# Kernel optimization log

Measured on AMD Instinct MI355X. Metric: run time of the kernel, lower is better.

Reference implementation:

```python
import jax, jax.numpy as jnp
import numpy as np

N_ETYPES = 4


def setup_inputs() -> dict:
    key = jax.random.key(0)
    ks = jax.random.split(key, 6)
    N, E, F = 50000, 800000, 128
    x = jax.random.normal(ks[0], (N, F), dtype=jnp.float32)
    edge_index = jax.random.randint(ks[1], (2, E), 0, N, dtype=jnp.int64)
    edge_type = jax.random.randint(ks[2], (E,), 0, N_ETYPES, dtype=jnp.int64)
    scale = 1.0 / np.sqrt(F)
    W_self = jax.random.normal(ks[3], (N_ETYPES, F, F), dtype=jnp.float32) * scale
    W_neigh = jax.random.normal(ks[4], (N_ETYPES, F, F), dtype=jnp.float32) * scale
    b = jnp.zeros((N_ETYPES, F), dtype=jnp.float32)
    return {"x": x, "edge_index": edge_index, "edge_type": edge_type,
            "W_self": W_self, "W_neigh": W_neigh, "b": b}


def reference(x, edge_index, edge_type, W_self, W_neigh, b):
    # HeteroConv: per-edge-type SageConv (mean aggregation), then mean over types.
    N = x.shape[0]
    src, dst = edge_index[0], edge_index[1]
    msg = x[src]                                   # [E, F] gathered source features
    outs = []
    for t in range(N_ETYPES):                      # small fixed loop over edge types
        w = (edge_type == t).astype(x.dtype)[:, None]          # [E, 1] type mask
        agg = jax.ops.segment_sum(msg * w, dst, num_segments=N)  # [N, F]
        cnt = jax.ops.segment_sum(w, dst, num_segments=N)        # [N, 1]
        mean_agg = agg / jnp.maximum(cnt, 1.0)
        outs.append(x @ W_self[t] + mean_agg @ W_neigh[t] + b[t])
    out = jnp.stack(outs, axis=0)                  # [n_etypes, N, F]
    return out.mean(axis=0)                        # reduction='mean' over edge types
```

## Files before the change

### kernel.cpp

```cpp
#include <hip/hip_runtime.h>

#define FDIM 128
#define NT 4
#define KDIM (FDIM * (NT + 1))
#define GBM 32

#define RSH 5
#define RNODES 32
#define RCAP 768
#define NBKT 128
#define CHUNK 4096

typedef __attribute__((ext_vector_type(8))) _Float16 h8v;
typedef __attribute__((ext_vector_type(4))) float f4v;

__device__ __forceinline__ unsigned short f2h(float f) {
    _Float16 h = (_Float16)f;
    return __builtin_bit_cast(unsigned short, h);
}
__device__ __forceinline__ void gload_lds16(const void* g, void* l) {
    __builtin_amdgcn_global_load_lds(
        (const __attribute__((address_space(1))) unsigned int*)g,
        (__attribute__((address_space(3))) unsigned int*)l, 16, 0, 0);
}

__global__ __launch_bounds__(256) void x2h(const float* __restrict__ x,
                                           unsigned short* __restrict__ xh, int n4) {
    int i = blockIdx.x * blockDim.x + threadIdx.x;
    if (i < n4) {
        float4 v = reinterpret_cast<const float4*>(x)[i];
        ushort4 o;
        o.x = f2h(v.x);
        o.y = f2h(v.y);
        o.z = f2h(v.z);
        o.w = f2h(v.w);
        reinterpret_cast<ushort4*>(xh)[i] = o;
    }
}

__global__ void mix_weights(const float* __restrict__ Wself,
                            const float* __restrict__ Wneigh,
                            const float* __restrict__ b,
                            unsigned short* __restrict__ WmixT,
                            float* __restrict__ bmean) {
    int i = blockIdx.x * blockDim.x + threadIdx.x;
    if (i >= KDIM * FDIM) return;
    int k = i / FDIM, j = i % FDIM;
    float v;
    if (k < FDIM) {
        v = 0.25f * (Wself[(size_t)(0 * FDIM + k) * FDIM + j] +
                     Wself[(size_t)(1 * FDIM + k) * FDIM + j] +
                     Wself[(size_t)(2 * FDIM + k) * FDIM + j] +
                     Wself[(size_t)(3 * FDIM + k) * FDIM + j]);
    } else {
        int t = (k - FDIM) >> 7;
        int kk = (k - FDIM) & (FDIM - 1);
        v = 0.25f * Wneigh[((size_t)t * FDIM + kk) * FDIM + j];
    }
    WmixT[(size_t)j * KDIM + k] = f2h(v);
    if (i < FDIM) {
        bmean[i] = 0.25f * (b[i] + b[FDIM + i] + b[2 * FDIM + i] + b[3 * FDIM + i]);
    }
}

__global__ __launch_bounds__(256) void k_bin(
    const int* __restrict__ ei, const int* __restrict__ et,
    int* __restrict__ cur, unsigned int* __restrict__ bin,
    int N, int E, int NR) {
    __shared__ int lcnt[2048];
    __shared__ int lpos[2048];
    const int tid = threadIdx.x;
    const int e0 = blockIdx.x * CHUNK;

    for (int b = tid; b < NR; b += 256) lcnt[b] = 0;
    __syncthreads();

    int rs[16];
    unsigned int recs[16];
#pragma unroll
    for (int i = 0; i < 16; ++i) {
        int e = e0 + i * 256 + tid;
        if (e < E) {
            int src = ei[e];
            int dst = ei[E + e];
            int t = et[e];
            rs[i] = dst >> RSH;
            recs[i] = (unsigned int)src |
                      ((unsigned int)(dst & (RNODES - 1)) << 16) |
                      ((unsigned int)t << 21);
            atomicAdd(&lcnt[rs[i]], 1);
        } else {
            rs[i] = -1;
            recs[i] = 0;
        }
    }
    __syncthreads();

    for (int b = tid; b < NR; b += 256) {
        int c = lcnt[b];
        lpos[b] = (c > 0) ? atomicAdd(&cur[b * 16], c) : 0;
    }
    __syncthreads();

#pragma unroll
    for (int i = 0; i < 16; ++i) {
        if (rs[i] >= 0) {
            int p = atomicAdd(&lpos[rs[i]], 1);
            if (p < RCAP) bin[(size_t)rs[i] * RCAP + p] = recs[i];
        }
    }
}

__global__ __launch_bounds__(256) void k_fused(
    const unsigned short* __restrict__ xh, const int* __restrict__ cur,
    const unsigned int* __restrict__ bin, const unsigned short* __restrict__ WmixT,
    const float* __restrict__ bmean, float* __restrict__ out, int N) {
    __shared__ __align__(16) char smem[18944];
    unsigned int* recs   = (unsigned int*)smem;
    int* scanb           = (int*)(smem + 3072);
    int* cur2            = (int*)(smem + 3584);
    unsigned short* As   = (unsigned short*)smem;
    unsigned short* magg = (unsigned short*)smem;
    unsigned short* srcs = (unsigned short*)(smem + 8192);
    int* cnts            = (int*)(smem + 9728);
    int* boff            = (int*)(smem + 10240);
    unsigned short* Bs   = (unsigned short*)(smem + 10752);

    const int r = blockIdx.x;
    const int tid = threadIdx.x;

    int K = cur[r * 16];
    if (K > RCAP) K = RCAP;
    for (int i = tid; i < K; i += 256) recs[i] = bin[(size_t)r * RCAP + i];
    if (tid < NBKT) cnts[tid] = 0;
    __syncthreads();
    for (int i = tid; i < K; i += 256) {
        unsigned int rec = recs[i];
        int b = ((rec >> 21) << 5) | ((rec >> 16) & 31);
        atomicAdd(&cnts[b], 1);
    }
    __syncthreads();
    int v = (tid < NBKT) ? cnts[tid] : 0;
    if (tid < NBKT) scanb[tid] = v;
    __syncthreads();
    for (int off = 1; off < NBKT; off <<= 1) {
        int tv = (tid >= off && tid < NBKT) ? scanb[tid - off] : 0;
        __syncthreads();
        if (tid < NBKT) scanb[tid] += tv;
        __syncthreads();
    }
    if (tid < NBKT) { boff[tid] = scanb[tid] - v; cur2[tid] = scanb[tid] - v; }
    __syncthreads();
    for (int i = tid; i < K; i += 256) {
        unsigned int rec = recs[i];
        int b = ((rec >> 21) << 5) | ((rec >> 16) & 31);
        int p = atomicAdd(&cur2[b], 1);
        srcs[p] = (unsigned short)(rec & 0xffffu);
    }

    const int wid = tid >> 6, lane = tid & 63;
    const int wr = wid >> 1, wc = wid & 1;
    const int n0 = r * GBM;
    const int r16 = lane & 15, kg = lane >> 4;
    const int g = tid >> 4, ln = tid & 15;

    f4v acc[4];
#pragma unroll
    for (int n = 0; n < 4; ++n) acc[n] = (f4v){0.f, 0.f, 0.f, 0.f};
    __syncthreads();

#pragma unroll 1
    for (int ks = 0; ks < 4; ++ks) {
        int k0 = ks * 32;
        if (wid < 2) {
            int row = tid >> 2, c = tid & 3;
            int cs = c ^ ((row >> 1) & 3);
            int rg = n0 + row; if (rg >= N) rg = N - 1;
            gload_lds16(xh + (size_t)rg * FDIM + k0 + cs * 8, &As[wid * 512]);
        }
#pragma unroll
        for (int p = 0; p < 2; ++p) {
            int ck = p * 256 + tid;
            int col = ck >> 2, c = ck & 3;
            int cs = c ^ ((col >> 1) & 3);
            gload_lds16(WmixT + (size_t)col * KDIM + k0 + cs * 8,
                        &Bs[(p * 4 + wid) * 512]);
        }
        __syncthreads();
        h8v af, bfr[4];
        {
            int row = wr * 16 + r16;
            af = *reinterpret_cast<const h8v*>(
                &As[row * 32 + ((kg ^ ((row >> 1) & 3)) << 3)]);
        }
#pragma unroll
        for (int n = 0; n < 4; ++n) {
            int col = wc * 64 + n * 16 + r16;
            bfr[n] = *reinterpret_cast<const h8v*>(
                &Bs[col * 32 + ((kg ^ ((col >> 1) & 3)) << 3)]);
        }
#pragma unroll
        for (int n = 0; n < 4; ++n)
            acc[n] = __builtin_amdgcn_mfma_f32_16x16x32_f16(af, bfr[n], acc[n], 0, 0, 0);
        __syncthreads();
    }

#pragma unroll 1
    for (int t = 0; t < 4; ++t) {
#pragma unroll 1
        for (int it = 0; it < 2; ++it) {
            int dl = it * 16 + g;
            int b = (t << 5) | dl;
            int dst = n0 + dl;
            if (dst < N) {
                int beg = boff[b], m = cnts[b];
                h8v a0 = (h8v)(_Float16)0.f, a1 = (h8v)(_Float16)0.f;
                h8v a2 = (h8v)(_Float16)0.f, a3 = (h8v)(_Float16)0.f;
                int i = 0;
                for (; i + 4 <= m; i += 4) {
                    int s0 = srcs[beg + i], s1 = srcs[beg + i + 1];
                    int s2 = srcs[beg + i + 2], s3 = srcs[beg + i + 3];
                    a0 += *reinterpret_cast<const h8v*>(xh + (size_t)s0 * FDIM + ln * 8);
                    a1 += *reinterpret_cast<const h8v*>(xh + (size_t)s1 * FDIM + ln * 8);
                    a2 += *reinterpret_cast<const h8v*>(xh + (size_t)s2 * FDIM + ln * 8);
                    a3 += *reinterpret_cast<const h8v*>(xh + (size_t)s3 * FDIM + ln * 8);
                }
                if (i + 2 <= m) {
                    int s0 = srcs[beg + i], s1 = srcs[beg + i + 1];
                    a0 += *reinterpret_cast<const h8v*>(xh + (size_t)s0 * FDIM + ln * 8);
                    a1 += *reinterpret_cast<const h8v*>(xh + (size_t)s1 * FDIM + ln * 8);
                    i += 2;
                }
                if (i < m) {
                    int s0 = srcs[beg + i];
                    a0 += *reinterpret_cast<const h8v*>(xh + (size_t)s0 * FDIM + ln * 8);
                }
                float rc = (m > 0) ? 1.0f / (float)m : 0.0f;
                h8v o = ((a0 + a1) + (a2 + a3)) * (_Float16)rc;
                *reinterpret_cast<h8v*>(&magg[dl * FDIM + ((ln ^ (dl & 15)) << 3)]) = o;
            }
        }
        __syncthreads();

#pragma unroll 1
        for (int ks = 0; ks < 4; ++ks) {
            int k0 = FDIM + t * FDIM + ks * 32;
#pragma unroll
            for (int p = 0; p < 2; ++p) {
                int ck = p * 256 + tid;
                int col = ck >> 2, c = ck & 3;
                int cs = c ^ ((col >> 1) & 3);
                gload_lds16(WmixT + (size_t)col * KDIM + k0 + cs * 8,
                            &Bs[(p * 4 + wid) * 512]);
            }
            __syncthreads();
            h8v af, bfr[4];
            {
                int row = wr * 16 + r16;
                af = *reinterpret_cast<const h8v*>(
                    &magg[row * FDIM + (((ks * 4 + kg) ^ (row & 15)) << 3)]);
            }
#pragma unroll
            for (int n = 0; n < 4; ++n) {
                int col = wc * 64 + n * 16 + r16;
                bfr[n] = *reinterpret_cast<const h8v*>(
                    &Bs[col * 32 + ((kg ^ ((col >> 1) & 3)) << 3)]);
            }
#pragma unroll
            for (int n = 0; n < 4; ++n)
                acc[n] = __builtin_amdgcn_mfma_f32_16x16x32_f16(af, bfr[n], acc[n], 0, 0, 0);
            __syncthreads();
        }
    }

    float bm[4];
#pragma unroll
    for (int n = 0; n < 4; ++n) bm[n] = bmean[wc * 64 + n * 16 + r16];
#pragma unroll
    for (int j = 0; j < 4; ++j) {
        int row = n0 + wr * 16 + kg * 4 + j;
        if (row < N) {
            float* o = out + (size_t)row * FDIM;
#pragma unroll
            for (int n = 0; n < 4; ++n)
                o[wc * 64 + n * 16 + r16] = acc[n][j] + bm[n];
        }
    }
}

extern "C" void kernel_launch(void* const* d_in, const int* in_sizes, int n_in,
                              void* d_out, int out_size, void* d_ws, size_t ws_size,
                              hipStream_t stream) {
    const float* x      = (const float*)d_in[0];
    const int*   ei     = (const int*)d_in[1];
    const int*   et     = (const int*)d_in[2];
    const float* Wself  = (const float*)d_in[3];
    const float* Wneigh = (const float*)d_in[4];
    const float* b      = (const float*)d_in[5];
    float* out = (float*)d_out;

    const int N = in_sizes[0] / FDIM;
    const int E = in_sizes[2];
    const int NR = (N + RNODES - 1) >> RSH;

    char* ws = (char*)d_ws;
    unsigned short* xh    = (unsigned short*)ws;
    unsigned short* WmixT = xh + (size_t)N * FDIM;
    float* bmean = (float*)(WmixT + (size_t)FDIM * KDIM);
    int* cur     = (int*)(bmean + FDIM);
    unsigned int* bin = (unsigned int*)(cur + (size_t)NR * 16);

    hipMemsetAsync(cur, 0, (size_t)NR * 16 * sizeof(int), stream);

    x2h<<<(N * FDIM / 4 + 255) / 256, 256, 0, stream>>>(x, xh, N * FDIM / 4);

    mix_weights<<<(KDIM * FDIM + 255) / 256, 256, 0, stream>>>(Wself, Wneigh, b, WmixT, bmean);

    k_bin<<<(E + CHUNK - 1) / CHUNK, 256, 0, stream>>>(ei, et, cur, bin, N, E, NR);

    k_fused<<<NR, 256, 0, stream>>>(xh, cur, bin, WmixT, bmean, out, N);
}
```

Measured before the change: 96.25 us.

## Merge prep kernels into one launch and use wave-shuffle bucket scan

The x-to-half conversion, weight mixing and edge binning kernels are merged into one launch that dispatches on block index, removing two kernel launches and letting the three independent prep jobs overlap on the GPU. The x conversion now handles eight elements per thread. In the fused kernel, the 128-bucket prefix scan is replaced by a single-wave shuffle scan with two buckets per lane, which drops several block-wide barriers. The merged kernel reserves the binning kernel's shared-memory footprint for every block, which may reduce occupancy for the conversion blocks.

```diff
diff --git a/kernel.cpp b/kernel.cpp
--- a/kernel.cpp
+++ b/kernel.cpp
@@ -24,89 +24,82 @@
         (__attribute__((address_space(3))) unsigned int*)l, 16, 0, 0);
 }
 
-__global__ __launch_bounds__(256) void x2h(const float* __restrict__ x,
-                                           unsigned short* __restrict__ xh, int n4) {
-    int i = blockIdx.x * blockDim.x + threadIdx.x;
-    if (i < n4) {
-        float4 v = reinterpret_cast<const float4*>(x)[i];
-        ushort4 o;
-        o.x = f2h(v.x);
-        o.y = f2h(v.y);
-        o.z = f2h(v.z);
-        o.w = f2h(v.w);
-        reinterpret_cast<ushort4*>(xh)[i] = o;
-    }
-}
-
-__global__ void mix_weights(const float* __restrict__ Wself,
-                            const float* __restrict__ Wneigh,
-                            const float* __restrict__ b,
-                            unsigned short* __restrict__ WmixT,
-                            float* __restrict__ bmean) {
-    int i = blockIdx.x * blockDim.x + threadIdx.x;
-    if (i >= KDIM * FDIM) return;
-    int k = i / FDIM, j = i % FDIM;
-    float v;
-    if (k < FDIM) {
-        v = 0.25f * (Wself[(size_t)(0 * FDIM + k) * FDIM + j] +
-                     Wself[(size_t)(1 * FDIM + k) * FDIM + j] +
-                     Wself[(size_t)(2 * FDIM + k) * FDIM + j] +
-                     Wself[(size_t)(3 * FDIM + k) * FDIM + j]);
-    } else {
-        int t = (k - FDIM) >> 7;
-        int kk = (k - FDIM) & (FDIM - 1);
-        v = 0.25f * Wneigh[((size_t)t * FDIM + kk) * FDIM + j];
-    }
-    WmixT[(size_t)j * KDIM + k] = f2h(v);
-    if (i < FDIM) {
-        bmean[i] = 0.25f * (b[i] + b[FDIM + i] + b[2 * FDIM + i] + b[3 * FDIM + i]);
-    }
-}
-
-__global__ __launch_bounds__(256) void k_bin(
-    const int* __restrict__ ei, const int* __restrict__ et,
-    int* __restrict__ cur, unsigned int* __restrict__ bin,
-    int N, int E, int NR) {
+__global__ __launch_bounds__(256) void k_prep(
+    const float* __restrict__ x, const int* __restrict__ ei,
+    const int* __restrict__ et, const float* __restrict__ Wself,
+    const float* __restrict__ Wneigh, const float* __restrict__ bvec,
+    unsigned short* __restrict__ xh, unsigned short* __restrict__ WmixT,
+    float* __restrict__ bmean, int* __restrict__ cur,
+    unsigned int* __restrict__ bin, int N, int E, int NR, int nbBin, int nbX) {
     __shared__ int lcnt[2048];
     __shared__ int lpos[2048];
+    const int bid = blockIdx.x;
     const int tid = threadIdx.x;
-    const int e0 = blockIdx.x * CHUNK;
-
-    for (int b = tid; b < NR; b += 256) lcnt[b] = 0;
-    __syncthreads();
-
-    int rs[16];
-    unsigned int recs[16];
-#pragma unroll
-    for (int i = 0; i < 16; ++i) {
-        int e = e0 + i * 256 + tid;
-        if (e < E) {
-            int src = ei[e];
-            int dst = ei[E + e];
-            int t = et[e];
-            rs[i] = dst >> RSH;
-            recs[i] = (unsigned int)src |
-                      ((unsigned int)(dst & (RNODES - 1)) << 16) |
-                      ((unsigned int)t << 21);
-            atomicAdd(&lcnt[rs[i]], 1);
-        } else {
-            rs[i] = -1;
-            recs[i] = 0;
-        }
-    }
-    __syncthreads();
-
-    for (int b = tid; b < NR; b += 256) {
-        int c = lcnt[b];
-        lpos[b] = (c > 0) ? atomicAdd(&cur[b * 16], c) : 0;
-    }
-    __syncthreads();
-
-#pragma unroll
-    for (int i = 0; i < 16; ++i) {
-        if (rs[i] >= 0) {
-            int p = atomicAdd(&lpos[rs[i]], 1);
-            if (p < RCAP) bin[(size_t)rs[i] * RCAP + p] = recs[i];
+
+    if (bid < nbBin) {
+        const int e0 = bid * CHUNK;
+        for (int b = tid; b < NR; b += 256) lcnt[b] = 0;
+        __syncthreads();
+        int rs[16];
+        unsigned int recs[16];
+#pragma unroll
+        for (int i = 0; i < 16; ++i) {
+            int e = e0 + i * 256 + tid;
+            if (e < E) {
+                int src = ei[e];
+                int dst = ei[E + e];
+                int t = et[e];
+                rs[i] = dst >> RSH;
+                recs[i] = (unsigned int)src |
+                          ((unsigned int)(dst & (RNODES - 1)) << 16) |
+                          ((unsigned int)t << 21);
+                atomicAdd(&lcnt[rs[i]], 1);
+            } else { rs[i] = -1; recs[i] = 0; }
+        }
+        __syncthreads();
+        for (int b = tid; b < NR; b += 256) {
+            int c = lcnt[b];
+            lpos[b] = (c > 0) ? atomicAdd(&cur[b * 16], c) : 0;
+        }
+        __syncthreads();
+#pragma unroll
+        for (int i = 0; i < 16; ++i) {
+            if (rs[i] >= 0) {
+                int p = atomicAdd(&lpos[rs[i]], 1);
+                if (p < RCAP) bin[(size_t)rs[i] * RCAP + p] = recs[i];
+            }
+        }
+    } else if (bid < nbBin + nbX) {
+        int i = (bid - nbBin) * 256 + tid;
+        int n8 = N * FDIM / 8;
+        if (i < n8) {
+            float4 v0 = reinterpret_cast<const float4*>(x)[i * 2];
+            float4 v1 = reinterpret_cast<const float4*>(x)[i * 2 + 1];
+            ushort4 o0, o1;
+            o0.x = f2h(v0.x); o0.y = f2h(v0.y); o0.z = f2h(v0.z); o0.w = f2h(v0.w);
+            o1.x = f2h(v1.x); o1.y = f2h(v1.y); o1.z = f2h(v1.z); o1.w = f2h(v1.w);
+            reinterpret_cast<ushort4*>(xh)[i * 2] = o0;
+            reinterpret_cast<ushort4*>(xh)[i * 2 + 1] = o1;
+        }
+    } else {
+        int i = (bid - nbBin - nbX) * 256 + tid;
+        if (i < KDIM * FDIM) {
+            int k = i / FDIM, j = i % FDIM;
+            float v;
+            if (k < FDIM) {
+                v = 0.25f * (Wself[(size_t)(0 * FDIM + k) * FDIM + j] +
+                             Wself[(size_t)(1 * FDIM + k) * FDIM + j] +
+                             Wself[(size_t)(2 * FDIM + k) * FDIM + j] +
+                             Wself[(size_t)(3 * FDIM + k) * FDIM + j]);
+            } else {
+                int t = (k - FDIM) >> 7;
+                int kk = (k - FDIM) & (FDIM - 1);
+                v = 0.25f * Wneigh[((size_t)t * FDIM + kk) * FDIM + j];
+            }
+            WmixT[(size_t)j * KDIM + k] = f2h(v);
+            if (i < FDIM)
+                bmean[i] = 0.25f * (bvec[i] + bvec[FDIM + i] +
+                                    bvec[2 * FDIM + i] + bvec[3 * FDIM + i]);
         }
     }
 }
@@ -117,7 +110,6 @@
     const float* __restrict__ bmean, float* __restrict__ out, int N) {
     __shared__ __align__(16) char smem[18944];
     unsigned int* recs   = (unsigned int*)smem;
-    int* scanb           = (int*)(smem + 3072);
     int* cur2            = (int*)(smem + 3584);
     unsigned short* As   = (unsigned short*)smem;
     unsigned short* magg = (unsigned short*)smem;
@@ -140,16 +132,20 @@
         atomicAdd(&cnts[b], 1);
     }
     __syncthreads();
-    int v = (tid < NBKT) ? cnts[tid] : 0;
-    if (tid < NBKT) scanb[tid] = v;
-    __syncthreads();
-    for (int off = 1; off < NBKT; off <<= 1) {
-        int tv = (tid >= off && tid < NBKT) ? scanb[tid - off] : 0;
-        __syncthreads();
-        if (tid < NBKT) scanb[tid] += tv;
-        __syncthreads();
-    }
-    if (tid < NBKT) { boff[tid] = scanb[tid] - v; cur2[tid] = scanb[tid] - v; }
+    if (tid < 64) {
+        int c0 = cnts[2 * tid], c1 = cnts[2 * tid + 1];
+        int tot = c0 + c1;
+        int xs = tot;
+        for (int off = 1; off < 64; off <<= 1) {
+            int y = __shfl_up(xs, off, 64);
+            if (tid >= off) xs += y;
+        }
+        int excl = xs - tot;
+        boff[2 * tid] = excl;
+        boff[2 * tid + 1] = excl + c0;
+        cur2[2 * tid] = excl;
+        cur2[2 * tid + 1] = excl + c0;
+    }
     __syncthreads();
     for (int i = tid; i < K; i += 256) {
         unsigned int rec = recs[i];
@@ -312,11 +308,13 @@
 
     hipMemsetAsync(cur, 0, (size_t)NR * 16 * sizeof(int), stream);
 
-    x2h<<<(N * FDIM / 4 + 255) / 256, 256, 0, stream>>>(x, xh, N * FDIM / 4);
-
-    mix_weights<<<(KDIM * FDIM + 255) / 256, 256, 0, stream>>>(Wself, Wneigh, b, WmixT, bmean);
-
-    k_bin<<<(E + CHUNK - 1) / CHUNK, 256, 0, stream>>>(ei, et, cur, bin, N, E, NR);
+    const int nbBin = (E + CHUNK - 1) / CHUNK;
+    const int nbX   = (N * FDIM / 8 + 255) / 256;
+    const int nbM   = (KDIM * FDIM + 255) / 256;
+
+    k_prep<<<nbBin + nbX + nbM, 256, 0, stream>>>(
+        x, ei, et, Wself, Wneigh, b, xh, WmixT, bmean, cur, bin,
+        N, E, NR, nbBin, nbX);
 
     k_fused<<<NR, 256, 0, stream>>>(xh, cur, bin, WmixT, bmean, out, N);
 }
```

Result: faster. 87.60 us (median of 2 runs) (-9.0%).
